# Optimization experiments

Hardware: AMD Instinct MI355X
Metric: run time of the kernel (lower is better)

Reference implementation:

```python
import jax, jax.numpy as jnp
import numpy as np

N = 5000        # nodes (repo uses 'sample/5000')
D_IN = 512      # feature dim
D_OUT = 16      # output_dim
K = 3           # num meta-paths
N_CLASSES = 100 # num_Labels
P_EDGE = 0.0064 # ~32 avg degree


def setup_inputs() -> dict:
    key = jax.random.key(0)
    ks = jax.random.split(key, 8)
    features = jax.random.normal(ks[0], (N, D_IN), dtype=jnp.float32)
    # sparse binary similarity matrices, symmetrized
    adj = (jax.random.uniform(ks[1], (K, N, N)) < P_EDGE).astype(jnp.float32)
    adj = jnp.maximum(adj, adj.transpose(0, 2, 1))
    W_gnn = jax.random.normal(ks[2], (K, D_IN, D_OUT), dtype=jnp.float32) / np.sqrt(D_IN).astype(np.float32)
    b_gnn = jnp.zeros((K, D_OUT), dtype=jnp.float32)
    att_w = jax.random.normal(ks[3], (K, 2 * D_OUT, 1), dtype=jnp.float32)  # as in torch.randn
    W_final = jax.random.normal(ks[4], (D_OUT, N_CLASSES), dtype=jnp.float32) / np.sqrt(D_OUT).astype(np.float32)
    b_final = jnp.zeros((N_CLASSES,), dtype=jnp.float32)
    return dict(features=features, adj=adj, W_gnn=W_gnn, b_gnn=b_gnn,
                att_w=att_w, W_final=W_final, b_final=b_final)


def _gcn_norm(A_bin):
    # GCNConv normalization: D^{-1/2} (A + I) D^{-1/2} with unit edge weights
    n = A_bin.shape[-1]
    Ahat = A_bin + jnp.eye(n, dtype=A_bin.dtype)
    dinv = jax.lax.rsqrt(Ahat.sum(-1))  # deg >= 1 due to self loops
    return dinv[..., :, None] * Ahat * dinv[..., None, :]


def reference(features, adj, W_gnn, b_gnn, att_w, W_final, b_final):
    # --- per-meta-path GCNConv (edge weights are all 1, from nonzero pattern) ---
    norm = _gcn_norm((adj != 0).astype(features.dtype))          # [K,N,N]
    XW = jnp.einsum('nd,kdo->kno', features, W_gnn)              # [K,N,Dout]
    h = jnp.einsum('knm,kmo->kno', norm, XW) + b_gnn[:, None, :]
    f_meta = jnp.max(h, axis=0)                                  # 'max' aggregation, [N,Dout]

    # --- pairwise attention over meta-paths (vectorized NxN loop) ---
    d = f_meta.shape[1]
    a = f_meta @ att_w[:, :d, 0].T   # [N,K] contribution of f_meta[i]
    b = f_meta @ att_w[:, d:, 0].T   # [N,K] contribution of f_meta[j]
    scores = jnp.exp(jax.nn.relu(a[:, None, :] + b[None, :, :]))  # [N,N,K]
    attn = scores / scores.sum(-1, keepdims=True)

    # --- fuse meta-path adjacencies ---
    A_meta = jnp.einsum('nmk,knm->nm', attn, adj)                # [N,N]

    # --- final GCNConv on the nonzero pattern of A_meta (unit edge weights) ---
    norm_meta = _gcn_norm((A_meta != 0).astype(features.dtype))
    predictions = norm_meta @ (f_meta @ W_final) + b_final
    return f_meta, A_meta, predictions
```

## Files before the change

kernel.cpp:

```cpp
#include <hip/hip_runtime.h>
#include <cstdint>
#include <cstddef>

#define N_NODES 5000
#define DIN 512
#define DOUT 16
#define KMP 3
#define NCLS 100
#define WSTRIDE 160
#define NWORDS 157
#define NQ 1250
#define CAPK 160
#define CAPU 320
#define NJT 313
#define NXW (KMP * NJT)

__global__ __launch_bounds__(256)
void kA(const float* __restrict__ adj, const float* __restrict__ feat,
        const float* __restrict__ Wg,
        uint32_t* __restrict__ planes, float* __restrict__ dinv,
        float* __restrict__ udinv,
        uint16_t* __restrict__ nbrK, int* __restrict__ cntK,
        uint16_t* __restrict__ nbrU, int* __restrict__ cntU,
        float* __restrict__ XW) {
    int bid = blockIdx.x;
    int t = threadIdx.x;

    if (bid >= N_NODES) {
        int b2 = bid - N_NODES;
        int k = b2 / NJT;
        int jt = b2 - k * NJT;
        int j = jt * 16 + (t >> 4);
        int o = t & 15;
        if (j < N_NODES) {
            const float4* f4 = (const float4*)(feat + (size_t)j * DIN);
            const float* wk = Wg + (size_t)k * DIN * DOUT + o;
            float acc = 0.f;
            #pragma unroll 4
            for (int d4 = 0; d4 < DIN / 4; ++d4) {
                float4 f = f4[d4];
                acc += f.x * wk[(4 * d4 + 0) * DOUT]
                     + f.y * wk[(4 * d4 + 1) * DOUT]
                     + f.z * wk[(4 * d4 + 2) * DOUT]
                     + f.w * wk[(4 * d4 + 3) * DOUT];
            }
            XW[((size_t)k * N_NODES + j) * DOUT + o] = acc;
        }
        return;
    }

    int i = bid;
    int lane = t & 63;
    int wv   = t >> 6;
    __shared__ uint32_t nib32[320];
    __shared__ int wtot[4];
    uint8_t* nib = (uint8_t*)nib32;
    uint32_t wsav[KMP];

    #pragma unroll
    for (int k = 0; k < KMP; ++k) {
        const float* arow = adj + ((size_t)k * N_NODES + i) * N_NODES;
        __syncthreads();
        #pragma unroll
        for (int it = 0; it < 5; ++it) {
            int q = it * 256 + t;
            uint32_t m = 0;
            if (q < NQ) {
                float4 v = *(const float4*)(arow + 4 * q);
                m = (v.x != 0.f ? 1u : 0u) | (v.y != 0.f ? 2u : 0u) |
                    (v.z != 0.f ? 4u : 0u) | (v.w != 0.f ? 8u : 0u);
            }
            nib[q] = (uint8_t)m;
        }
        __syncthreads();
        uint32_t word = 0;
        int cnt = 0;
        if (t < NWORDS) {
            uint32_t lo = nib32[2 * t], hi = nib32[2 * t + 1];
            word = (lo & 0xFu) | ((lo >> 4) & 0xF0u) | ((lo >> 8) & 0xF00u) | ((lo >> 12) & 0xF000u)
                 | ((hi << 16) & 0xF0000u) | ((hi << 12) & 0xF00000u)
                 | ((hi << 8) & 0xF000000u) | ((hi << 4) & 0xF0000000u);
            planes[((size_t)k * N_NODES + i) * WSTRIDE + t] = word;
            cnt = __popc(word);
        }
        wsav[k] = word;
        int x = cnt;
        #pragma unroll
        for (int s = 1; s < 64; s <<= 1) {
            int y = __shfl_up(x, s);
            if (lane >= s) x += y;
        }
        if (lane == 63) wtot[wv] = x;
        __syncthreads();
        int prefix = 0;
        #pragma unroll
        for (int w = 0; w < 4; ++w) if (w < wv) prefix += wtot[w];
        int total = wtot[0] + wtot[1] + wtot[2] + wtot[3];
        int pos = prefix + x - cnt;
        uint16_t* out = nbrK + ((size_t)k * N_NODES + i) * CAPK;
        uint32_t wtmp = word;
        while (wtmp) {
            int b = __builtin_ctz(wtmp);
            wtmp &= wtmp - 1;
            if (pos < CAPK) out[pos] = (uint16_t)(32 * t + b);
            ++pos;
        }
        if (t == 0) {
            dinv[k * N_NODES + i] = rsqrtf(1.0f + (float)total);
            cntK[k * N_NODES + i] = (total < CAPK) ? total : CAPK;
        }
    }

    __syncthreads();
    uint32_t uw = wsav[0] | wsav[1] | wsav[2];
    int cnt = __popc(uw);
    int x = cnt;
    #pragma unroll
    for (int s = 1; s < 64; s <<= 1) {
        int y = __shfl_up(x, s);
        if (lane >= s) x += y;
    }
    if (lane == 63) wtot[wv] = x;
    __syncthreads();
    int prefix = 0;
    #pragma unroll
    for (int w = 0; w < 4; ++w) if (w < wv) prefix += wtot[w];
    int total = wtot[0] + wtot[1] + wtot[2] + wtot[3];
    int pos = prefix + x - cnt;
    uint16_t* out = nbrU + (size_t)i * CAPU;
    while (uw) {
        int b = __builtin_ctz(uw);
        uw &= uw - 1;
        if (pos < CAPU) out[pos] = (uint16_t)(32 * t + b);
        ++pos;
    }
    if (t == 0) {
        cntU[i] = (total < CAPU) ? total : CAPU;
        udinv[i] = rsqrtf(1.0f + (float)total);
    }
}

__global__ void k34_fmeta_ab_gd(const uint16_t* __restrict__ nbrK, const int* __restrict__ cntK,
                                const float* __restrict__ XW, const float* __restrict__ dinv,
                                const float* __restrict__ bg, const float* __restrict__ aw,
                                const float* __restrict__ Wf, const float* __restrict__ udinv,
                                float* __restrict__ f_meta, float* __restrict__ a4,
                                float* __restrict__ b4, float* __restrict__ Gd) {
    int t = threadIdx.x;
    int o = t & 15;
    int r = t >> 4;
    int i = blockIdx.x * 4 + r;
    __shared__ float fs[4][17];
    float hmax = -1e30f;
    #pragma unroll
    for (int k = 0; k < KMP; ++k) {
        const float* xw = XW + (size_t)k * N_NODES * DOUT;
        const float* dv = dinv + (size_t)k * N_NODES;
        int row = k * N_NODES + i;
        int nn = cntK[row];
        const uint16_t* nb = nbrK + (size_t)row * CAPK;
        float di = dv[i];
        float a0 = di * xw[i * DOUT + o];
        float a1 = 0.f, a2 = 0.f, a3 = 0.f;
        int n = 0;
        for (; n + 4 <= nn; n += 4) {
            ushort4 jj = *(const ushort4*)(nb + n);
            a0 += dv[jj.x] * xw[(int)jj.x * DOUT + o];
            a1 += dv[jj.y] * xw[(int)jj.y * DOUT + o];
            a2 += dv[jj.z] * xw[(int)jj.z * DOUT + o];
            a3 += dv[jj.w] * xw[(int)jj.w * DOUT + o];
        }
        for (; n < nn; ++n) a0 += dv[nb[n]] * xw[(int)nb[n] * DOUT + o];
        float h = di * ((a0 + a1) + (a2 + a3)) + bg[k * DOUT + o];
        hmax = fmaxf(hmax, h);
    }
    f_meta[i * DOUT + o] = hmax;
    fs[r][o] = hmax;
    float sa0 = hmax * aw[0 * 32 + o], sb0 = hmax * aw[0 * 32 + 16 + o];
    float sa1 = hmax * aw[1 * 32 + o], sb1 = hmax * aw[1 * 32 + 16 + o];
    float sa2 = hmax * aw[2 * 32 + o], sb2 = hmax * aw[2 * 32 + 16 + o];
    #pragma unroll
    for (int s = 1; s < 16; s <<= 1) {
        sa0 += __shfl_xor(sa0, s, 16); sb0 += __shfl_xor(sb0, s, 16);
        sa1 += __shfl_xor(sa1, s, 16); sb1 += __shfl_xor(sb1, s, 16);
        sa2 += __shfl_xor(sa2, s, 16); sb2 += __shfl_xor(sb2, s, 16);
    }
    if (o < 4) {
        float sa = (o == 0) ? sa0 : (o == 1) ? sa1 : (o == 2) ? sa2 : 0.f;
        float sb = (o == 0) ? sb0 : (o == 1) ? sb1 : (o == 2) ? sb2 : 0.f;
        a4[i * 4 + o] = sa;
        b4[i * 4 + o] = sb;
    }
    __syncthreads();
    float f[DOUT];
    #pragma unroll
    for (int q = 0; q < DOUT; ++q) f[q] = fs[r][q];
    float ud = udinv[i];
    for (int c = o; c < NCLS; c += 16) {
        float acc = 0.f;
        #pragma unroll
        for (int q = 0; q < DOUT; ++q) acc += f[q] * Wf[q * NCLS + c];
        Gd[(size_t)i * NCLS + c] = acc * ud;
    }
}

__device__ __forceinline__ float attn_frac(float x0, float x1, float x2,
                                           uint32_t b0, uint32_t b1, uint32_t b2) {
    float e0 = __expf(fmaxf(x0, 0.f));
    float e1 = __expf(fmaxf(x1, 0.f));
    float e2 = __expf(fmaxf(x2, 0.f));
    float num = (b0 ? e0 : 0.f) + (b1 ? e1 : 0.f) + (b2 ? e2 : 0.f);
    return __fdividef(num, e0 + e1 + e2);
}

#define NB_K5 625

__global__ __launch_bounds__(256)
void kC(const uint32_t* __restrict__ planes,
        const float* __restrict__ a4, const float* __restrict__ b4,
        float* __restrict__ Am,
        const uint16_t* __restrict__ nbrU, const int* __restrict__ cntU,
        const float* __restrict__ Gd, const float* __restrict__ udinv,
        const float* __restrict__ bf, float* __restrict__ pred) {
    int bid = blockIdx.x;
    int t = threadIdx.x;

    if (bid < NB_K5) {
        int i0 = bid * 8;
        __shared__ float a_s[8][3];
        if (t < 24) { int r = t / 3, k = t % 3; a_s[r][k] = a4[(i0 + r) * 4 + k]; }
        __syncthreads();
        for (int c = 0; c < 5; ++c) {
            int j4 = 4 * (t + 256 * c);
            if (j4 >= N_NODES) break;
            int w = j4 >> 5, sh = j4 & 31;
            const float4* bp = (const float4*)(b4 + (size_t)j4 * 4);
            float4 bj0 = bp[0], bj1 = bp[1], bj2 = bp[2], bj3 = bp[3];
            #pragma unroll
            for (int r = 0; r < 8; ++r) {
                int i = i0 + r;
                uint32_t q0 = planes[(size_t)i * WSTRIDE + w] >> sh;
                uint32_t q1 = planes[(size_t)(N_NODES + i) * WSTRIDE + w] >> sh;
                uint32_t q2 = planes[(size_t)(2 * N_NODES + i) * WSTRIDE + w] >> sh;
                uint32_t un = (q0 | q1 | q2) & 0xFu;
                float4 outv = make_float4(0.f, 0.f, 0.f, 0.f);
                if (un) {
                    float A0 = a_s[r][0], A1 = a_s[r][1], A2 = a_s[r][2];
                    if (un & 1u) outv.x = attn_frac(A0 + bj0.x, A1 + bj0.y, A2 + bj0.z, q0 & 1u, q1 & 1u, q2 & 1u);
                    if (un & 2u) outv.y = attn_frac(A0 + bj1.x, A1 + bj1.y, A2 + bj1.z, q0 & 2u, q1 & 2u, q2 & 2u);
                    if (un & 4u) outv.z = attn_frac(A0 + bj2.x, A1 + bj2.y, A2 + bj2.z, q0 & 4u, q1 & 4u, q2 & 4u);
                    if (un & 8u) outv.w = attn_frac(A0 + bj3.x, A1 + bj3.y, A2 + bj3.z, q0 & 8u, q1 & 8u, q2 & 8u);
                }
                *(float4*)(Am + (size_t)i * N_NODES + j4) = outv;
            }
        }
    } else {
        int b2 = bid - NB_K5;
        int i = b2 * 2 + (t >> 7);
        int c = t & 127;
        if (c >= NCLS) return;
        int nn = cntU[i];
        const uint16_t* nb = nbrU + (size_t)i * CAPU;
        float a0 = Gd[(size_t)i * NCLS + c];
        float a1 = 0.f, a2 = 0.f, a3 = 0.f;
        int n = 0;
        for (; n + 4 <= nn; n += 4) {
            ushort4 jj = *(const ushort4*)(nb + n);
            a0 += Gd[(size_t)jj.x * NCLS + c];
            a1 += Gd[(size_t)jj.y * NCLS + c];
            a2 += Gd[(size_t)jj.z * NCLS + c];
            a3 += Gd[(size_t)jj.w * NCLS + c];
        }
        for (; n < nn; ++n) a0 += Gd[(size_t)nb[n] * NCLS + c];
        pred[(size_t)i * NCLS + c] = udinv[i] * ((a0 + a1) + (a2 + a3)) + bf[c];
    }
}

extern "C" void kernel_launch(void* const* d_in, const int* in_sizes, int n_in,
                              void* d_out, int out_size, void* d_ws, size_t ws_size,
                              hipStream_t stream) {
    const float* feat = (const float*)d_in[0];
    const float* adj  = (const float*)d_in[1];
    const float* Wg   = (const float*)d_in[2];
    const float* bg   = (const float*)d_in[3];
    const float* aw   = (const float*)d_in[4];
    const float* Wf   = (const float*)d_in[5];
    const float* bf   = (const float*)d_in[6];

    float* f_meta = (float*)d_out;
    float* Am     = f_meta + (size_t)N_NODES * DOUT;
    float* pred   = Am + (size_t)N_NODES * N_NODES;

    char* ws = (char*)d_ws;
    size_t off = 0;
    auto alloc = [&](size_t bytes) {
        void* p = ws + off;
        off = (off + bytes + 255) & ~(size_t)255;
        return p;
    };
    uint32_t* planes = (uint32_t*)alloc((size_t)KMP * N_NODES * WSTRIDE * 4);
    float* dinv  = (float*)alloc((size_t)KMP * N_NODES * 4);
    float* XW    = (float*)alloc((size_t)KMP * N_NODES * DOUT * 4);
    float* a4    = (float*)alloc((size_t)N_NODES * 16);
    float* b4    = (float*)alloc((size_t)N_NODES * 16);
    float* udinv = (float*)alloc((size_t)N_NODES * 4);
    float* Gd    = (float*)alloc((size_t)N_NODES * NCLS * 4);
    uint16_t* nbrK = (uint16_t*)alloc((size_t)KMP * N_NODES * CAPK * 2);
    int*      cntK = (int*)alloc((size_t)KMP * N_NODES * 4);
    uint16_t* nbrU = (uint16_t*)alloc((size_t)N_NODES * CAPU * 2);
    int*      cntU = (int*)alloc((size_t)N_NODES * 4);

    hipLaunchKernelGGL(kA, dim3(N_NODES + NXW), dim3(256), 0, stream,
                       adj, feat, Wg, planes, dinv, udinv, nbrK, cntK, nbrU, cntU, XW);
    hipLaunchKernelGGL(k34_fmeta_ab_gd, dim3(N_NODES / 4), dim3(64), 0, stream,
                       nbrK, cntK, XW, dinv, bg, aw, Wf, udinv, f_meta, a4, b4, Gd);
    hipLaunchKernelGGL(kC, dim3(NB_K5 + N_NODES / 2), dim3(256), 0, stream,
                       planes, a4, b4, Am, nbrU, cntU, Gd, udinv, bf, pred);
}
```

Baseline: 570.3 us.

## Batch adjacency loads across meta-paths, nontemporal streaming, and widen neighbor gather

kA now issues all three meta-path row loads up front with nontemporal loads into separate shared buffers and performs a single fused 4-way prefix scan, removing per-k barriers and serialized scans. The f_meta kernel now uses one 64-lane wave per node, splitting the neighbor list across four sub-groups with shuffle reductions, to raise parallelism in the gather. The A_meta output write becomes a nontemporal store so the large dense result does not pollute the cache. Shared memory usage in kA grows and the batched loads raise register pressure.

```diff
diff --git a/kernel.cpp b/kernel.cpp
--- a/kernel.cpp
+++ b/kernel.cpp
@@ -14,6 +14,8 @@
 #define CAPU 320
 #define NJT 313
 #define NXW (KMP * NJT)
+
+typedef float f32x4 __attribute__((ext_vector_type(4)));
 
 __global__ __launch_bounds__(256)
 void kA(const float* __restrict__ adj, const float* __restrict__ feat,
@@ -52,105 +54,111 @@
     int i = bid;
     int lane = t & 63;
     int wv   = t >> 6;
-    __shared__ uint32_t nib32[320];
-    __shared__ int wtot[4];
-    uint8_t* nib = (uint8_t*)nib32;
-    uint32_t wsav[KMP];
-
+    __shared__ uint32_t nib32[KMP][320];
+    __shared__ int wtot[4][4];
+
+    #pragma unroll
+    for (int it = 0; it < 15; ++it) {
+        const int k  = it / 5;
+        const int ql = (it - 5 * k) * 256 + t;
+        uint32_t m = 0;
+        if (ql < NQ) {
+            const f32x4* arow4 = (const f32x4*)(adj + ((size_t)k * N_NODES + i) * N_NODES);
+            f32x4 v = __builtin_nontemporal_load(arow4 + ql);
+            m = (v.x != 0.f ? 1u : 0u) | (v.y != 0.f ? 2u : 0u) |
+                (v.z != 0.f ? 4u : 0u) | (v.w != 0.f ? 8u : 0u);
+        }
+        ((uint8_t*)nib32[k])[ql] = (uint8_t)m;
+    }
+    __syncthreads();
+
+    uint32_t w[4];
+    int cnt[4];
     #pragma unroll
     for (int k = 0; k < KMP; ++k) {
-        const float* arow = adj + ((size_t)k * N_NODES + i) * N_NODES;
-        __syncthreads();
-        #pragma unroll
-        for (int it = 0; it < 5; ++it) {
-            int q = it * 256 + t;
-            uint32_t m = 0;
-            if (q < NQ) {
-                float4 v = *(const float4*)(arow + 4 * q);
-                m = (v.x != 0.f ? 1u : 0u) | (v.y != 0.f ? 2u : 0u) |
-                    (v.z != 0.f ? 4u : 0u) | (v.w != 0.f ? 8u : 0u);
-            }
-            nib[q] = (uint8_t)m;
-        }
-        __syncthreads();
         uint32_t word = 0;
-        int cnt = 0;
         if (t < NWORDS) {
-            uint32_t lo = nib32[2 * t], hi = nib32[2 * t + 1];
+            uint32_t lo = nib32[k][2 * t], hi = nib32[k][2 * t + 1];
             word = (lo & 0xFu) | ((lo >> 4) & 0xF0u) | ((lo >> 8) & 0xF00u) | ((lo >> 12) & 0xF000u)
                  | ((hi << 16) & 0xF0000u) | ((hi << 12) & 0xF00000u)
                  | ((hi << 8) & 0xF000000u) | ((hi << 4) & 0xF0000000u);
             planes[((size_t)k * N_NODES + i) * WSTRIDE + t] = word;
-            cnt = __popc(word);
-        }
-        wsav[k] = word;
-        int x = cnt;
+        }
+        w[k] = word;
+        cnt[k] = __popc(word);
+    }
+    w[3] = w[0] | w[1] | w[2];
+    cnt[3] = __popc(w[3]);
+
+    int x[4];
+    #pragma unroll
+    for (int q = 0; q < 4; ++q) x[q] = cnt[q];
+    #pragma unroll
+    for (int s = 1; s < 64; s <<= 1) {
+        int y0 = __shfl_up(x[0], s), y1 = __shfl_up(x[1], s);
+        int y2 = __shfl_up(x[2], s), y3 = __shfl_up(x[3], s);
+        if (lane >= s) { x[0] += y0; x[1] += y1; x[2] += y2; x[3] += y3; }
+    }
+    if (lane == 63) {
+        wtot[0][wv] = x[0]; wtot[1][wv] = x[1];
+        wtot[2][wv] = x[2]; wtot[3][wv] = x[3];
+    }
+    __syncthreads();
+
+    #pragma unroll
+    for (int q = 0; q < 4; ++q) {
+        int prefix = 0, total = 0;
         #pragma unroll
-        for (int s = 1; s < 64; s <<= 1) {
-            int y = __shfl_up(x, s);
-            if (lane >= s) x += y;
-        }
-        if (lane == 63) wtot[wv] = x;
-        __syncthreads();
-        int prefix = 0;
-        #pragma unroll
-        for (int w = 0; w < 4; ++w) if (w < wv) prefix += wtot[w];
-        int total = wtot[0] + wtot[1] + wtot[2] + wtot[3];
-        int pos = prefix + x - cnt;
-        uint16_t* out = nbrK + ((size_t)k * N_NODES + i) * CAPK;
-        uint32_t wtmp = word;
-        while (wtmp) {
-            int b = __builtin_ctz(wtmp);
-            wtmp &= wtmp - 1;
-            if (pos < CAPK) out[pos] = (uint16_t)(32 * t + b);
-            ++pos;
-        }
-        if (t == 0) {
-            dinv[k * N_NODES + i] = rsqrtf(1.0f + (float)total);
-            cntK[k * N_NODES + i] = (total < CAPK) ? total : CAPK;
-        }
-    }
-
-    __syncthreads();
-    uint32_t uw = wsav[0] | wsav[1] | wsav[2];
-    int cnt = __popc(uw);
-    int x = cnt;
-    #pragma unroll
-    for (int s = 1; s < 64; s <<= 1) {
-        int y = __shfl_up(x, s);
-        if (lane >= s) x += y;
-    }
-    if (lane == 63) wtot[wv] = x;
-    __syncthreads();
-    int prefix = 0;
-    #pragma unroll
-    for (int w = 0; w < 4; ++w) if (w < wv) prefix += wtot[w];
-    int total = wtot[0] + wtot[1] + wtot[2] + wtot[3];
-    int pos = prefix + x - cnt;
-    uint16_t* out = nbrU + (size_t)i * CAPU;
-    while (uw) {
-        int b = __builtin_ctz(uw);
-        uw &= uw - 1;
-        if (pos < CAPU) out[pos] = (uint16_t)(32 * t + b);
-        ++pos;
-    }
-    if (t == 0) {
-        cntU[i] = (total < CAPU) ? total : CAPU;
-        udinv[i] = rsqrtf(1.0f + (float)total);
-    }
-}
-
-__global__ void k34_fmeta_ab_gd(const uint16_t* __restrict__ nbrK, const int* __restrict__ cntK,
-                                const float* __restrict__ XW, const float* __restrict__ dinv,
-                                const float* __restrict__ bg, const float* __restrict__ aw,
-                                const float* __restrict__ Wf, const float* __restrict__ udinv,
-                                float* __restrict__ f_meta, float* __restrict__ a4,
-                                float* __restrict__ b4, float* __restrict__ Gd) {
+        for (int wq = 0; wq < 4; ++wq) {
+            int v = wtot[q][wq];
+            total += v;
+            if (wq < wv) prefix += v;
+        }
+        int pos = prefix + x[q] - cnt[q];
+        uint32_t word = w[q];
+        if (q < KMP) {
+            uint16_t* out = nbrK + ((size_t)q * N_NODES + i) * CAPK;
+            while (word) {
+                int b = __builtin_ctz(word);
+                word &= word - 1;
+                if (pos < CAPK) out[pos] = (uint16_t)(32 * t + b);
+                ++pos;
+            }
+            if (t == 0) {
+                dinv[q * N_NODES + i] = rsqrtf(1.0f + (float)total);
+                cntK[q * N_NODES + i] = (total < CAPK) ? total : CAPK;
+            }
+        } else {
+            uint16_t* out = nbrU + (size_t)i * CAPU;
+            while (word) {
+                int b = __builtin_ctz(word);
+                word &= word - 1;
+                if (pos < CAPU) out[pos] = (uint16_t)(32 * t + b);
+                ++pos;
+            }
+            if (t == 0) {
+                cntU[i] = (total < CAPU) ? total : CAPU;
+                udinv[i] = rsqrtf(1.0f + (float)total);
+            }
+        }
+    }
+}
+
+__global__ __launch_bounds__(256)
+void k34_fmeta_ab_gd(const uint16_t* __restrict__ nbrK, const int* __restrict__ cntK,
+                     const float* __restrict__ XW, const float* __restrict__ dinv,
+                     const float* __restrict__ bg, const float* __restrict__ aw,
+                     const float* __restrict__ Wf, const float* __restrict__ udinv,
+                     float* __restrict__ f_meta, float* __restrict__ a4,
+                     float* __restrict__ b4, float* __restrict__ Gd) {
     int t = threadIdx.x;
-    int o = t & 15;
-    int r = t >> 4;
-    int i = blockIdx.x * 4 + r;
+    int wv = t >> 6;
+    int lane = t & 63;
+    int o = lane & 15;
+    int s = lane >> 4;
+    int i = blockIdx.x * 4 + wv;
     __shared__ float fs[4][17];
+
     float hmax = -1e30f;
     #pragma unroll
     for (int k = 0; k < KMP; ++k) {
@@ -160,43 +168,48 @@
         int nn = cntK[row];
         const uint16_t* nb = nbrK + (size_t)row * CAPK;
         float di = dv[i];
-        float a0 = di * xw[i * DOUT + o];
-        float a1 = 0.f, a2 = 0.f, a3 = 0.f;
-        int n = 0;
-        for (; n + 4 <= nn; n += 4) {
-            ushort4 jj = *(const ushort4*)(nb + n);
+        float a0 = 0.f, a1 = 0.f, a2 = 0.f, a3 = 0.f;
+        for (int n0 = 4 * s; n0 < nn; n0 += 16) {
+            ushort4 jj = *(const ushort4*)(nb + n0);
             a0 += dv[jj.x] * xw[(int)jj.x * DOUT + o];
-            a1 += dv[jj.y] * xw[(int)jj.y * DOUT + o];
-            a2 += dv[jj.z] * xw[(int)jj.z * DOUT + o];
-            a3 += dv[jj.w] * xw[(int)jj.w * DOUT + o];
-        }
-        for (; n < nn; ++n) a0 += dv[nb[n]] * xw[(int)nb[n] * DOUT + o];
-        float h = di * ((a0 + a1) + (a2 + a3)) + bg[k * DOUT + o];
+            if (n0 + 1 < nn) a1 += dv[jj.y] * xw[(int)jj.y * DOUT + o];
+            if (n0 + 2 < nn) a2 += dv[jj.z] * xw[(int)jj.z * DOUT + o];
+            if (n0 + 3 < nn) a3 += dv[jj.w] * xw[(int)jj.w * DOUT + o];
+        }
+        float red = (a0 + a1) + (a2 + a3);
+        red += __shfl_xor(red, 16);
+        red += __shfl_xor(red, 32);
+        red += di * xw[i * DOUT + o];
+        float h = di * red + bg[k * DOUT + o];
         hmax = fmaxf(hmax, h);
     }
-    f_meta[i * DOUT + o] = hmax;
-    fs[r][o] = hmax;
+    if (s == 0) {
+        f_meta[i * DOUT + o] = hmax;
+        fs[wv][o] = hmax;
+    }
+    __syncthreads();
+
     float sa0 = hmax * aw[0 * 32 + o], sb0 = hmax * aw[0 * 32 + 16 + o];
     float sa1 = hmax * aw[1 * 32 + o], sb1 = hmax * aw[1 * 32 + 16 + o];
     float sa2 = hmax * aw[2 * 32 + o], sb2 = hmax * aw[2 * 32 + 16 + o];
     #pragma unroll
-    for (int s = 1; s < 16; s <<= 1) {
-        sa0 += __shfl_xor(sa0, s, 16); sb0 += __shfl_xor(sb0, s, 16);
-        sa1 += __shfl_xor(sa1, s, 16); sb1 += __shfl_xor(sb1, s, 16);
-        sa2 += __shfl_xor(sa2, s, 16); sb2 += __shfl_xor(sb2, s, 16);
-    }
-    if (o < 4) {
+    for (int sh = 1; sh < 16; sh <<= 1) {
+        sa0 += __shfl_xor(sa0, sh, 16); sb0 += __shfl_xor(sb0, sh, 16);
+        sa1 += __shfl_xor(sa1, sh, 16); sb1 += __shfl_xor(sb1, sh, 16);
+        sa2 += __shfl_xor(sa2, sh, 16); sb2 += __shfl_xor(sb2, sh, 16);
+    }
+    if (s == 0 && o < 4) {
         float sa = (o == 0) ? sa0 : (o == 1) ? sa1 : (o == 2) ? sa2 : 0.f;
         float sb = (o == 0) ? sb0 : (o == 1) ? sb1 : (o == 2) ? sb2 : 0.f;
         a4[i * 4 + o] = sa;
         b4[i * 4 + o] = sb;
     }
-    __syncthreads();
+
     float f[DOUT];
     #pragma unroll
-    for (int q = 0; q < DOUT; ++q) f[q] = fs[r][q];
+    for (int q = 0; q < DOUT; ++q) f[q] = fs[wv][q];
     float ud = udinv[i];
-    for (int c = o; c < NCLS; c += 16) {
+    for (int c = lane; c < NCLS; c += 64) {
         float acc = 0.f;
         #pragma unroll
         for (int q = 0; q < DOUT; ++q) acc += f[q] * Wf[q * NCLS + c];
@@ -243,7 +256,7 @@
                 uint32_t q1 = planes[(size_t)(N_NODES + i) * WSTRIDE + w] >> sh;
                 uint32_t q2 = planes[(size_t)(2 * N_NODES + i) * WSTRIDE + w] >> sh;
                 uint32_t un = (q0 | q1 | q2) & 0xFu;
-                float4 outv = make_float4(0.f, 0.f, 0.f, 0.f);
+                f32x4 outv = (f32x4)(0.f);
                 if (un) {
                     float A0 = a_s[r][0], A1 = a_s[r][1], A2 = a_s[r][2];
                     if (un & 1u) outv.x = attn_frac(A0 + bj0.x, A1 + bj0.y, A2 + bj0.z, q0 & 1u, q1 & 1u, q2 & 1u);
@@ -251,7 +264,7 @@
                     if (un & 4u) outv.z = attn_frac(A0 + bj2.x, A1 + bj2.y, A2 + bj2.z, q0 & 4u, q1 & 4u, q2 & 4u);
                     if (un & 8u) outv.w = attn_frac(A0 + bj3.x, A1 + bj3.y, A2 + bj3.z, q0 & 8u, q1 & 8u, q2 & 8u);
                 }
-                *(float4*)(Am + (size_t)i * N_NODES + j4) = outv;
+                __builtin_nontemporal_store(outv, (f32x4*)(Am + (size_t)i * N_NODES + j4));
             }
         }
     } else {
@@ -312,7 +325,7 @@
 
     hipLaunchKernelGGL(kA, dim3(N_NODES + NXW), dim3(256), 0, stream,
                        adj, feat, Wg, planes, dinv, udinv, nbrK, cntK, nbrU, cntU, XW);
-    hipLaunchKernelGGL(k34_fmeta_ab_gd, dim3(N_NODES / 4), dim3(64), 0, stream,
+    hipLaunchKernelGGL(k34_fmeta_ab_gd, dim3(N_NODES / 4), dim3(256), 0, stream,
                        nbrK, cntK, XW, dinv, bg, aw, Wf, udinv, f_meta, a4, b4, Gd);
     hipLaunchKernelGGL(kC, dim3(NB_K5 + N_NODES / 2), dim3(256), 0, stream,
                        planes, a4, b4, Am, nbrU, cntU, Gd, udinv, bf, pred);
```

Result: faster. 532.1 us (-6.7%).
